# Kernel optimization log

Measured on AMD Instinct MI355X. Metric: run time of the kernel, lower is better.

Reference implementation:

```python
import jax, jax.numpy as jnp
import numpy as np

N = 100_000      # nodes
E = 1_600_000    # edges (avg degree 16)
H = 128          # hidden_channels == num_node_features
L = 6            # SAGEConv layers (third=True)
G = 128          # graphs in batch (for global_mean_pool)
C = 10           # num_classes
EPS = 1e-5       # BatchNorm eps


def setup_inputs() -> dict:
    key = jax.random.key(0)
    ks = jax.random.split(key, 8)
    s = 1.0 / np.sqrt(H)
    x = jax.random.normal(ks[0], (N, H), jnp.float32)
    edge_index = jax.random.randint(ks[1], (2, E), 0, N, dtype=jnp.int32)
    batch = jnp.sort(jax.random.randint(ks[2], (N,), 0, G, dtype=jnp.int32))
    return {
        "x": x,
        "edge_index": edge_index,
        "batch": batch,
        "Wl": jax.random.normal(ks[3], (L, H, H), jnp.float32) * s,  # neighbor lin
        "bl": jnp.zeros((L, H), jnp.float32),
        "Wr": jax.random.normal(ks[4], (L, H, H), jnp.float32) * s,  # root lin (no bias)
        "gamma": jnp.ones((L, H), jnp.float32),
        "beta": jnp.zeros((L, H), jnp.float32),
        "lin_W": jax.random.normal(ks[5], (H, C), jnp.float32) * s,
        "lin_b": jnp.zeros((C,), jnp.float32),
    }


def reference(x, edge_index, batch, Wl, bl, Wr, gamma, beta, lin_W, lin_b):
    src, dst = edge_index[0], edge_index[1]
    n = x.shape[0]
    # in-degree for mean aggregation (constant across layers)
    deg = jax.ops.segment_sum(jnp.ones((src.shape[0],), x.dtype), dst, num_segments=n)
    inv_deg = jnp.where(deg > 0, 1.0 / deg, 0.0)[:, None]  # [n,1]

    for l in range(Wl.shape[0]):
        # SAGEConv: lin_l(mean_{j->i} x_j) + lin_r(x_i)
        agg = jax.ops.segment_sum(x[src], dst, num_segments=n) * inv_deg  # [n,H]
        h = agg @ Wl[l] + bl[l] + x @ Wr[l]
        # BatchNorm1d (training-style batch stats, biased variance)
        mu = jnp.mean(h, axis=0)
        var = jnp.mean((h - mu) ** 2, axis=0)
        h = (h - mu) * jax.lax.rsqrt(var + EPS) * gamma[l] + beta[l]
        x = jax.nn.relu(h)

    # global_mean_pool over graph ids
    cnt = jax.ops.segment_sum(jnp.ones((n,), x.dtype), batch, num_segments=G)
    pooled = jax.ops.segment_sum(x, batch, num_segments=G) / jnp.maximum(cnt, 1.0)[:, None]
    # dropout(p=0.5) is identity in eval mode
    return pooled @ lin_W + lin_b  # [G, C]
```

## Files before the change

### kernel.cpp

```cpp
#include <hip/hip_runtime.h>
#include <hip/hip_bf16.h>

#define N_NODES 100000
#define N_EDGES 1600000
#define HDIM    128
#define NLAYER  6
#define NGRAPH  128
#define NCLASS  10
#define BN_EPS  1e-5f

#define POOL_SPLIT 16

#define NBUCK   196
#define BSH     9
#define KC_BLOCKS 250
#define KC_CHUNK  6400
#define LCOL_CAP  10240

#define GBM 128
#define NBLK_G ((N_NODES + GBM - 1) / GBM)

typedef __attribute__((ext_vector_type(8))) short short8v;
typedef __attribute__((ext_vector_type(4))) float f32x4;
typedef __attribute__((ext_vector_type(2))) float f32x2;
typedef __attribute__((ext_vector_type(4))) int int4v;
typedef __attribute__((ext_vector_type(2))) int int2v;

__device__ __forceinline__ float b2f(unsigned short h) {
    return __uint_as_float(((unsigned int)h) << 16);
}
__device__ __forceinline__ unsigned short f2b(float f) {
    unsigned int u = __float_as_uint(f);
    u += 0x7FFF + ((u >> 16) & 1);
    return (unsigned short)(u >> 16);
}
__device__ __forceinline__ void gl_lds16(const void* g, void* l) {
    __builtin_amdgcn_global_load_lds((const __attribute__((address_space(1))) unsigned int*)g,
                                     (__attribute__((address_space(3))) unsigned int*)l,
                                     16, 0, 0);
}
__device__ __forceinline__ short8v bn_pack(short8v v, float4 scA, float4 scB,
                                           float4 shA, float4 shB) {
    short8v o;
    o[0] = (short)f2b(fmaxf(0.f, b2f((unsigned short)v[0]) * scA.x + shA.x));
    o[1] = (short)f2b(fmaxf(0.f, b2f((unsigned short)v[1]) * scA.y + shA.y));
    o[2] = (short)f2b(fmaxf(0.f, b2f((unsigned short)v[2]) * scA.z + shA.z));
    o[3] = (short)f2b(fmaxf(0.f, b2f((unsigned short)v[3]) * scA.w + shA.w));
    o[4] = (short)f2b(fmaxf(0.f, b2f((unsigned short)v[4]) * scB.x + shB.x));
    o[5] = (short)f2b(fmaxf(0.f, b2f((unsigned short)v[5]) * scB.y + shB.y));
    o[6] = (short)f2b(fmaxf(0.f, b2f((unsigned short)v[6]) * scB.z + shB.z));
    o[7] = (short)f2b(fmaxf(0.f, b2f((unsigned short)v[7]) * scB.w + shB.w));
    return o;
}


__global__ void __launch_bounds__(256) k_hist(const int* __restrict__ dst,
                                              int* __restrict__ bcnt) {
    __shared__ int h[NBUCK];
    for (int i = threadIdx.x; i < NBUCK; i += 256) h[i] = 0;
    __syncthreads();
    const int4v* d4 = (const int4v*)dst;
    int base = blockIdx.x * (KC_CHUNK / 4);
    for (int i = threadIdx.x; i < KC_CHUNK / 4; i += 256) {
        int4v d = __builtin_nontemporal_load(d4 + base + i);
        atomicAdd(&h[d[0] >> BSH], 1);
        atomicAdd(&h[d[1] >> BSH], 1);
        atomicAdd(&h[d[2] >> BSH], 1);
        atomicAdd(&h[d[3] >> BSH], 1);
    }
    __syncthreads();
    for (int i = threadIdx.x; i < NBUCK; i += 256)
        if (h[i]) atomicAdd(&bcnt[i], h[i]);
}

__global__ void k_bscan(const int* __restrict__ bcnt, int* __restrict__ boff,
                        int* __restrict__ bcur, int* __restrict__ row_off) {
    if (threadIdx.x == 0 && blockIdx.x == 0) {
        int acc = 0;
        for (int i = 0; i < NBUCK; ++i) {
            boff[i] = acc; bcur[i] = acc; acc += bcnt[i];
        }
        boff[NBUCK] = acc;
        row_off[N_NODES] = N_EDGES;
    }
}

__global__ void __launch_bounds__(256) k_part(const int* __restrict__ src,
                                              const int* __restrict__ dst,
                                              int* __restrict__ bcur,
                                              int2v* __restrict__ P) {
    __shared__ int h[NBUCK];
    __shared__ int gbase[NBUCK];
    for (int i = threadIdx.x; i < NBUCK; i += 256) h[i] = 0;
    __syncthreads();
    const int4v* d4 = (const int4v*)dst;
    const int4v* s4 = (const int4v*)src;
    const int base = blockIdx.x * (KC_CHUNK / 4);
    for (int i = threadIdx.x; i < KC_CHUNK / 4; i += 256) {
        int4v d = __builtin_nontemporal_load(d4 + base + i);
        atomicAdd(&h[d[0] >> BSH], 1);
        atomicAdd(&h[d[1] >> BSH], 1);
        atomicAdd(&h[d[2] >> BSH], 1);
        atomicAdd(&h[d[3] >> BSH], 1);
    }
    __syncthreads();
    for (int i = threadIdx.x; i < NBUCK; i += 256) {
        int c = h[i];
        gbase[i] = c ? atomicAdd(&bcur[i], c) : 0;
        h[i] = 0;
    }
    __syncthreads();
    for (int i = threadIdx.x; i < KC_CHUNK / 4; i += 256) {
        int4v d = __builtin_nontemporal_load(d4 + base + i);
        int4v s = __builtin_nontemporal_load(s4 + base + i);
#pragma unroll
        for (int k = 0; k < 4; ++k) {
            int b = d[k] >> BSH;
            int pos = gbase[b] + atomicAdd(&h[b], 1);
            int2v pr; pr[0] = s[k]; pr[1] = d[k];
            P[pos] = pr;
        }
    }
}

__global__ void __launch_bounds__(1024) k_bucket(const int2v* __restrict__ P,
                                                 const int* __restrict__ boff,
                                                 int* __restrict__ row_off,
                                                 int* __restrict__ col) {
    __shared__ int ldeg[512];
    __shared__ int lcur[512];
    __shared__ int lcol[LCOL_CAP];
    const int tid = threadIdx.x;
    const int b = blockIdx.x;
    const int pbeg = boff[b], pend = boff[b + 1];
    const int nE = pend - pbeg;
    const int n0 = b << BSH;
    if (tid < 512) ldeg[tid] = 0;
    __syncthreads();
    for (int i = tid; i < nE; i += 1024) {
        int2v pr = P[pbeg + i];
        atomicAdd(&ldeg[pr[1] - n0], 1);
    }
    __syncthreads();
    int myd = (tid < 512) ? ldeg[tid] : 0;
    for (int off = 1; off < 512; off <<= 1) {
        int t = 0;
        if (tid < 512 && tid >= off) t = ldeg[tid - off];
        __syncthreads();
        if (tid < 512) ldeg[tid] += t;
        __syncthreads();
    }
    if (tid < 512) {
        int excl = ldeg[tid] - myd;
        lcur[tid] = excl;
        int node = n0 + tid;
        if (node < N_NODES) row_off[node] = pbeg + excl;
    }
    __syncthreads();
    for (int i = tid; i < nE; i += 1024) {
        int2v pr = P[pbeg + i];
        int pos = atomicAdd(&lcur[pr[1] - n0], 1);
        if (pos < LCOL_CAP) lcol[pos] = pr[0];
    }
    __syncthreads();
    for (int i = tid; i < nE; i += 1024) col[pbeg + i] = lcol[i];
}


__global__ void __launch_bounds__(256) k_cvt_x(const float* __restrict__ x,
                                               unsigned short* __restrict__ Xb,
                                               unsigned int* __restrict__ X8) {
    int idx = blockIdx.x * 256 + threadIdx.x;
    f32x4 v = __builtin_nontemporal_load(((const f32x4*)x) + idx);
    ushort4 o = { f2b(v[0]), f2b(v[1]), f2b(v[2]), f2b(v[3]) };
    ((ushort4*)Xb)[idx] = o;
    unsigned int d = 0;
    d = __builtin_amdgcn_cvt_pk_fp8_f32(v[0], v[1], d, false);
    d = __builtin_amdgcn_cvt_pk_fp8_f32(v[2], v[3], d, true);
    X8[idx] = d;
}

__global__ void __launch_bounds__(256) k_cvt_w(const float* __restrict__ Wl,
                                               const float* __restrict__ Wr,
                                               unsigned short* __restrict__ Wtb) {
    int idx = blockIdx.x * 256 + threadIdx.x;
    int kk = idx & 255;
    int n  = (idx >> 8) & 127;
    int l  = idx >> 15;
    float v = (kk < HDIM) ? Wl[l * HDIM * HDIM + kk * HDIM + n]
                          : Wr[l * HDIM * HDIM + (kk - HDIM) * HDIM + n];
    Wtb[idx] = f2b(v);
}

__global__ void __launch_bounds__(256) k_bnx8(const unsigned short* __restrict__ Hb,
                                              const float* __restrict__ scsh,
                                              int2v* __restrict__ X8) {
    int idx = blockIdx.x * 256 + threadIdx.x;
    int c8 = (idx & 15) * 8;
    short8v v = ((const short8v*)Hb)[idx];
    float f[8];
#pragma unroll
    for (int j = 0; j < 8; ++j)
        f[j] = fmaxf(0.f, b2f((unsigned short)v[j]) * scsh[c8 + j] + scsh[HDIM + c8 + j]);
    unsigned int d0 = 0, d1 = 0;
    d0 = __builtin_amdgcn_cvt_pk_fp8_f32(f[0], f[1], d0, false);
    d0 = __builtin_amdgcn_cvt_pk_fp8_f32(f[2], f[3], d0, true);
    d1 = __builtin_amdgcn_cvt_pk_fp8_f32(f[4], f[5], d1, false);
    d1 = __builtin_amdgcn_cvt_pk_fp8_f32(f[6], f[7], d1, true);
    int2v o; o[0] = (int)d0; o[1] = (int)d1;
    X8[idx] = o;
}


__global__ void __launch_bounds__(256) k_agg8(const unsigned char* __restrict__ X8,
                                              const int* __restrict__ row_off,
                                              const int* __restrict__ col,
                                              unsigned short* __restrict__ AGGb) {
    __shared__ int lcol[4096];
    __shared__ int sro[33];
    const int tid = threadIdx.x;
    const int nb0 = blockIdx.x * 32;
    if (tid <= 32) sro[tid] = row_off[nb0 + tid];
    __syncthreads();
    const int s0 = sro[0];
    const int nE = sro[32] - s0;
    const bool fits = (nE <= 4096);
    if (fits) {
        for (int i = tid; i < nE; i += 256) lcol[i] = col[s0 + i];
    }
    __syncthreads();

    const int g   = tid >> 3;
    const int c16 = (tid & 7) * 16;
    const int s = sro[g] - s0, e = sro[g + 1] - s0;
    const int* cp = fits ? lcol : (col + s0);

    f32x2 a2[8] = {};
    auto accum = [&](int4v v) {
#pragma unroll
        for (int q = 0; q < 4; ++q) {
            unsigned int w = (unsigned int)v[q];
            a2[2 * q]     += __builtin_amdgcn_cvt_pk_f32_fp8(w, false);
            a2[2 * q + 1] += __builtin_amdgcn_cvt_pk_f32_fp8(w, true);
        }
    };

    int p = s;
    for (; p + 8 <= e; p += 8) {
        int nbx[8];
#pragma unroll
        for (int j = 0; j < 8; ++j) nbx[j] = cp[p + j];
        int4v v[8];
#pragma unroll
        for (int j = 0; j < 8; ++j)
            v[j] = *(const int4v*)(X8 + (size_t)nbx[j] * HDIM + c16);
#pragma unroll
        for (int j = 0; j < 8; ++j) accum(v[j]);
    }
    if (p + 4 <= e) {
        int nbx[4];
#pragma unroll
        for (int j = 0; j < 4; ++j) nbx[j] = cp[p + j];
        int4v v[4];
#pragma unroll
        for (int j = 0; j < 4; ++j)
            v[j] = *(const int4v*)(X8 + (size_t)nbx[j] * HDIM + c16);
#pragma unroll
        for (int j = 0; j < 4; ++j) accum(v[j]);
        p += 4;
    }
    for (; p < e; ++p) {
        int4v v0 = *(const int4v*)(X8 + (size_t)cp[p] * HDIM + c16);
        accum(v0);
    }

    float w = (e > s) ? 1.0f / (float)(e - s) : 0.f;
    short8v o0, o1;
#pragma unroll
    for (int j = 0; j < 8; ++j) o0[j] = (short)f2b(a2[j >> 1][j & 1] * w);
#pragma unroll
    for (int j = 0; j < 8; ++j) o1[j] = (short)f2b(a2[4 + (j >> 1)][j & 1] * w);
    unsigned short* dst = AGGb + (size_t)(nb0 + g) * HDIM + c16;
    *(short8v*)dst = o0;
    *(short8v*)(dst + 8) = o1;
}


__global__ void __launch_bounds__(512) k_gemm_l0(const unsigned short* __restrict__ AGGb,
                                                 const unsigned short* __restrict__ Xb,
                                                 const unsigned short* __restrict__ Wtb,
                                                 const float* __restrict__ bl,
                                                 unsigned short* __restrict__ Hb,
                                                 float* __restrict__ pstat) {
    __shared__ __align__(16) char smem[32768];
    const int tid  = threadIdx.x;
    const int bm   = blockIdx.x * GBM;
    const int wv   = tid >> 6;
    const int lane = tid & 63;
    const int li   = lane & 15, hi = lane >> 4;
    const int wm   = wv & 1, wn = wv >> 1;

    f32x4 acc[4][2] = {};
    const int rr = tid >> 2, sk = tid & 3;
    const int swz = ((sk ^ ((rr >> 1) & 3)) << 4);

    auto stage = [&](int b, int step) {
        const unsigned short* Asrc = (step < 4) ? AGGb : Xb;
        const int kk0 = (step & 3) * 32;
        {
            int row = bm + rr; if (row >= N_NODES) row = N_NODES - 1;
            gl_lds16((const char*)(Asrc + (size_t)row * HDIM + kk0) + swz,
                     smem + b * 8192 + wv * 1024);
        }
        const int k0 = step * 32;
        gl_lds16((const char*)(Wtb + (size_t)rr * 256 + k0) + swz,
                 smem + 16384 + b * 8192 + wv * 1024);
    };

    stage(0, 0);
    __syncthreads();

    int buf = 0;
    for (int step = 0; step < 8; ++step) {
        if (step < 7) stage(buf ^ 1, step + 1);
        char* bA = smem + buf * 8192;
        char* bW = smem + 16384 + buf * 8192;
        short8v afr[4], bfr[2];
#pragma unroll
        for (int m = 0; m < 4; ++m) {
            int r = wm * 64 + m * 16 + li;
            afr[m] = *(const short8v*)(bA + r * 64 + ((hi ^ ((r >> 1) & 3)) << 4));
        }
#pragma unroll
        for (int nf = 0; nf < 2; ++nf) {
            int n = wn * 32 + nf * 16 + li;
            bfr[nf] = *(const short8v*)(bW + n * 64 + ((hi ^ ((n >> 1) & 3)) << 4));
        }
#pragma unroll
        for (int m = 0; m < 4; ++m)
#pragma unroll
            for (int nf = 0; nf < 2; ++nf)
                acc[m][nf] = __builtin_amdgcn_mfma_f32_16x16x32_bf16(afr[m], bfr[nf],
                                                                     acc[m][nf], 0, 0, 0);
        __syncthreads();
        buf ^= 1;
    }

    float* st = (float*)smem;
#pragma unroll
    for (int nf = 0; nf < 2; ++nf) {
        int c = wn * 32 + nf * 16 + li;
        float bb = bl[c];
        float ls = 0.f, lq = 0.f;
#pragma unroll
        for (int m = 0; m < 4; ++m) {
            int row0 = bm + wm * 64 + m * 16 + hi * 4;
#pragma unroll
            for (int j = 0; j < 4; ++j) {
                int row = row0 + j;
                if (row < N_NODES) {
                    float v = acc[m][nf][j] + bb;
                    Hb[(size_t)row * HDIM + c] = f2b(v);
                    ls += v; lq += v * v;
                }
            }
        }
        ls += __shfl_xor(ls, 16); ls += __shfl_xor(ls, 32);
        lq += __shfl_xor(lq, 16); lq += __shfl_xor(lq, 32);
        if (hi == 0) {
            st[wv * 128 + c] = ls;
            st[1024 + wv * 128 + c] = lq;
        }
    }
    __syncthreads();
    if (tid < 128) {
        int w0 = (tid >> 5) * 2;
        float s = st[w0 * 128 + tid] + st[(w0 + 1) * 128 + tid];
        pstat[blockIdx.x * 256 + tid] = s;
    } else if (tid < 256) {
        int c = tid - 128;
        int w0 = (c >> 5) * 2;
        float q = st[1024 + w0 * 128 + c] + st[1024 + (w0 + 1) * 128 + c];
        pstat[blockIdx.x * 256 + tid] = q;
    }
}

__global__ void __launch_bounds__(512) k_gemm_fuse(const unsigned short* __restrict__ AGGb,
                                                   const unsigned short* __restrict__ Hprev,
                                                   const float* __restrict__ scsh,
                                                   const unsigned short* __restrict__ Wtb,
                                                   const float* __restrict__ bl,
                                                   unsigned short* __restrict__ Hb,
                                                   float* __restrict__ pstat) {
    __shared__ __align__(16) char smem[32768];
    const int tid  = threadIdx.x;
    const int bm   = blockIdx.x * GBM;
    const int wv   = tid >> 6;
    const int lane = tid & 63;
    const int li   = lane & 15, hi = lane >> 4;
    const int wm   = wv & 1, wn = wv >> 1;

    f32x4 acc[4][2] = {};
    const int rr = tid >> 2, sk = tid & 3;
    const int swz = ((sk ^ ((rr >> 1) & 3)) << 4);

    auto stageW = [&](int b, int step) {
        const int k0 = step * 32;
        gl_lds16((const char*)(Wtb + (size_t)rr * 256 + k0) + swz,
                 smem + 16384 + b * 8192 + wv * 1024);
    };
    auto stageA = [&](int b, int step) {
        const int kk0 = step * 32;
        int row = bm + rr; if (row >= N_NODES) row = N_NODES - 1;
        gl_lds16((const char*)(AGGb + (size_t)row * HDIM + kk0) + swz,
                 smem + b * 8192 + wv * 1024);
    };

    stageA(0, 0); stageW(0, 0);
    __syncthreads();

    int buf = 0;
    for (int step = 0; step < 8; ++step) {
        char* curA = smem + buf * 8192;
        char* curW = smem + 16384 + buf * 8192;
        char* nxtA = smem + (buf ^ 1) * 8192;
        const int ns = step + 1;
        short8v rv;
        int c0 = 0;
        bool regstage = false;
        if (step < 7) {
            stageW(buf ^ 1, ns);
            if (ns < 4) {
                stageA(buf ^ 1, ns);
            } else {
                regstage = true;
                c0 = (ns - 4) * 32 + sk * 8;
                int row = bm + rr; if (row >= N_NODES) row = N_NODES - 1;
                rv = *(const short8v*)(Hprev + (size_t)row * HDIM + c0);
            }
        }

        short8v afr[4], bfr[2];
#pragma unroll
        for (int m = 0; m < 4; ++m) {
            int r = wm * 64 + m * 16 + li;
            afr[m] = *(const short8v*)(curA + r * 64 + ((hi ^ ((r >> 1) & 3)) << 4));
        }
#pragma unroll
        for (int nf = 0; nf < 2; ++nf) {
            int n = wn * 32 + nf * 16 + li;
            bfr[nf] = *(const short8v*)(curW + n * 64 + ((hi ^ ((n >> 1) & 3)) << 4));
        }
#pragma unroll
        for (int m = 0; m < 4; ++m)
#pragma unroll
            for (int nf = 0; nf < 2; ++nf)
                acc[m][nf] = __builtin_amdgcn_mfma_f32_16x16x32_bf16(afr[m], bfr[nf],
                                                                     acc[m][nf], 0, 0, 0);

        if (regstage) {
            float4 scA = *(const float4*)&scsh[c0];
            float4 scB = *(const float4*)&scsh[c0 + 4];
            float4 shA = *(const float4*)&scsh[HDIM + c0];
            float4 shB = *(const float4*)&scsh[HDIM + c0 + 4];
            *(short8v*)(nxtA + rr * 64 + swz) = bn_pack(rv, scA, scB, shA, shB);
        }
        __syncthreads();
        buf ^= 1;
    }

    float* st = (float*)smem;
#pragma unroll
    for (int nf = 0; nf < 2; ++nf) {
        int c = wn * 32 + nf * 16 + li;
        float bb = bl[c];
        float ls = 0.f, lq = 0.f;
#pragma unroll
        for (int m = 0; m < 4; ++m) {
            int row0 = bm + wm * 64 + m * 16 + hi * 4;
#pragma unroll
            for (int j = 0; j < 4; ++j) {
                int row = row0 + j;
                if (row < N_NODES) {
                    float v = acc[m][nf][j] + bb;
                    Hb[(size_t)row * HDIM + c] = f2b(v);
                    ls += v; lq += v * v;
                }
            }
        }
        ls += __shfl_xor(ls, 16); ls += __shfl_xor(ls, 32);
        lq += __shfl_xor(lq, 16); lq += __shfl_xor(lq, 32);
        if (hi == 0) {
            st[wv * 128 + c] = ls;
            st[1024 + wv * 128 + c] = lq;
        }
    }
    __syncthreads();
    if (tid < 128) {
        int w0 = (tid >> 5) * 2;
        float s = st[w0 * 128 + tid] + st[(w0 + 1) * 128 + tid];
        pstat[blockIdx.x * 256 + tid] = s;
    } else if (tid < 256) {
        int c = tid - 128;
        int w0 = (c >> 5) * 2;
        float q = st[1024 + w0 * 128 + c] + st[1024 + (w0 + 1) * 128 + c];
        pstat[blockIdx.x * 256 + tid] = q;
    }
}


__global__ void __launch_bounds__(256) k_red1(const float* __restrict__ pstat,
                                              float* __restrict__ red32) {
    int c = threadIdx.x, b = blockIdx.x;
    float s = 0.f;
    for (int r = b; r < NBLK_G; r += 32) s += pstat[r * 256 + c];
    red32[b * 256 + c] = s;
}

__global__ void __launch_bounds__(128) k_stats_final(const float* __restrict__ red32,
                                                     const float* __restrict__ gamma,
                                                     const float* __restrict__ beta,
                                                     float* __restrict__ scsh) {
    int c = threadIdx.x;
    float s = 0.f, q = 0.f;
    for (int r = 0; r < 32; ++r) { s += red32[r * 256 + c]; q += red32[r * 256 + 128 + c]; }
    float mu = s / (float)N_NODES;
    float var = q / (float)N_NODES - mu * mu;
    float rs = rsqrtf(var + BN_EPS);
    float sc = gamma[c] * rs;
    scsh[c] = sc;
    scsh[HDIM + c] = beta[c] - mu * sc;
}


__global__ void k_gbound(const int* __restrict__ batch, int* __restrict__ gb) {
    int t = blockIdx.x * 64 + threadIdx.x;
    if (t > NGRAPH) return;
    int lo = 0, hi = N_NODES;
    while (lo < hi) { int mid = (lo + hi) >> 1; if (batch[mid] < t) lo = mid + 1; else hi = mid; }
    gb[t] = lo;
}

__global__ void __launch_bounds__(128) k_pool_part(const unsigned short* __restrict__ Hb,
                                                   const float* __restrict__ scsh,
                                                   const int* __restrict__ gb,
                                                   float* __restrict__ ppart) {
    int g = blockIdx.x, sp = blockIdx.y;
    int c = threadIdx.x;
    float sc = scsh[c], sh = scsh[HDIM + c];
    int s = gb[g], e = gb[g + 1];
    float acc = 0.f;
    for (int i = s + sp; i < e; i += POOL_SPLIT)
        acc += fmaxf(0.f, b2f(Hb[(size_t)i * HDIM + c]) * sc + sh);
    ppart[(g * POOL_SPLIT + sp) * HDIM + c] = acc;
}

__global__ void __launch_bounds__(128) k_pool_final(const int* __restrict__ gb,
                                                    const float* __restrict__ ppart,
                                                    float* __restrict__ pooled) {
    int g = blockIdx.x, c = threadIdx.x;
    float s = 0.f;
    for (int sp = 0; sp < POOL_SPLIT; ++sp) s += ppart[(g * POOL_SPLIT + sp) * HDIM + c];
    int cnt = gb[g + 1] - gb[g]; if (cnt < 1) cnt = 1;
    pooled[g * HDIM + c] = s / (float)cnt;
}

__global__ void __launch_bounds__(128) k_lin(const float* __restrict__ pooled,
                                             const float* __restrict__ W,
                                             const float* __restrict__ bvec,
                                             float* __restrict__ out) {
    __shared__ float p[HDIM];
    int g = blockIdx.x, t = threadIdx.x;
    p[t] = pooled[g * HDIM + t];
    __syncthreads();
    if (t < NCLASS) {
        float acc = bvec[t];
        for (int k = 0; k < HDIM; ++k) acc += p[k] * W[k * NCLASS + t];
        out[g * NCLASS + t] = acc;
    }
}


extern "C" void kernel_launch(void* const* d_in, const int* in_sizes, int n_in,
                              void* d_out, int out_size, void* d_ws, size_t ws_size,
                              hipStream_t stream) {
    const float* x     = (const float*)d_in[0];
    const int*   eidx  = (const int*)d_in[1];
    const int*   batch = (const int*)d_in[2];
    const float* Wl    = (const float*)d_in[3];
    const float* bl    = (const float*)d_in[4];
    const float* Wr    = (const float*)d_in[5];
    const float* gamma = (const float*)d_in[6];
    const float* beta  = (const float*)d_in[7];
    const float* linW  = (const float*)d_in[8];
    const float* linb  = (const float*)d_in[9];
    float* out = (float*)d_out;

    const int* src = eidx;
    const int* dst = eidx + N_EDGES;

    char* p = (char*)d_ws;
    auto alloc = [&](size_t bytes) { char* r = p; p += (bytes + 255) & ~(size_t)255; return r; };
    unsigned short* Xb   = (unsigned short*)alloc((size_t)N_NODES * HDIM * 2);
    unsigned char*  X8   = (unsigned char*)alloc((size_t)N_NODES * HDIM);
    unsigned short* AGGb = (unsigned short*)alloc((size_t)N_NODES * HDIM * 2);
    unsigned short* HbA  = (unsigned short*)alloc((size_t)N_NODES * HDIM * 2);
    unsigned short* HbB  = (unsigned short*)alloc((size_t)N_NODES * HDIM * 2);
    unsigned short* Wtb  = (unsigned short*)alloc((size_t)NLAYER * 2 * HDIM * HDIM * 2);
    int*   row_off = (int*)alloc((N_NODES + 2) * 4);
    int*   col     = (int*)alloc((size_t)N_EDGES * 4);
    int2v* P       = (int2v*)alloc((size_t)N_EDGES * 8);
    int*   bcnt    = (int*)alloc(NBUCK * 4);
    int*   boff    = (int*)alloc((NBUCK + 1) * 4);
    int*   bcur    = (int*)alloc(NBUCK * 4);
    int*   gb      = (int*)alloc((NGRAPH + 2) * 4);
    float* pstat   = (float*)alloc((size_t)NBLK_G * 256 * 4);
    float* red32   = (float*)alloc(32 * 256 * 4);
    float* scsh    = (float*)alloc(2 * HDIM * 4);
    float* ppart   = (float*)alloc((size_t)NGRAPH * POOL_SPLIT * HDIM * 4);
    float* pooled  = (float*)alloc(NGRAPH * HDIM * 4);

    hipMemsetAsync(bcnt, 0, NBUCK * sizeof(int), stream);
    k_hist<<<KC_BLOCKS, 256, 0, stream>>>(dst, bcnt);
    k_bscan<<<1, 64, 0, stream>>>(bcnt, boff, bcur, row_off);
    k_part<<<KC_BLOCKS, 256, 0, stream>>>(src, dst, bcur, P);
    k_bucket<<<NBUCK, 1024, 0, stream>>>(P, boff, row_off, col);

    k_cvt_x<<<N_NODES * HDIM / 4 / 256, 256, 0, stream>>>(x, Xb, (unsigned int*)X8);
    k_cvt_w<<<NLAYER * 2 * HDIM * HDIM / 256, 256, 0, stream>>>(Wl, Wr, Wtb);
    k_gbound<<<3, 64, 0, stream>>>(batch, gb);

    k_agg8<<<N_NODES / 32, 256, 0, stream>>>(X8, row_off, col, AGGb);
    k_gemm_l0<<<NBLK_G, 512, 0, stream>>>(AGGb, Xb, Wtb, bl, HbA, pstat);
    k_red1<<<32, 256, 0, stream>>>(pstat, red32);
    k_stats_final<<<1, 128, 0, stream>>>(red32, gamma, beta, scsh);

    unsigned short* Hcur = HbA;
    for (int l = 1; l < NLAYER; ++l) {
        unsigned short* Hout = (l & 1) ? HbB : HbA;
        k_bnx8<<<N_NODES * HDIM / 8 / 256, 256, 0, stream>>>(Hcur, scsh, (int2v*)X8);
        k_agg8<<<N_NODES / 32, 256, 0, stream>>>(X8, row_off, col, AGGb);
        k_gemm_fuse<<<NBLK_G, 512, 0, stream>>>(
            AGGb, Hcur, scsh, Wtb + (size_t)l * 2 * HDIM * HDIM, bl + (size_t)l * HDIM,
            Hout, pstat);
        k_red1<<<32, 256, 0, stream>>>(pstat, red32);
        k_stats_final<<<1, 128, 0, stream>>>(red32, gamma + (size_t)l * HDIM,
                                             beta + (size_t)l * HDIM, scsh);
        Hcur = Hout;
    }

    k_pool_part<<<dim3(NGRAPH, POOL_SPLIT), 128, 0, stream>>>(Hcur, scsh, gb, ppart);
    k_pool_final<<<NGRAPH, 128, 0, stream>>>(gb, ppart, pooled);
    k_lin<<<NGRAPH, 128, 0, stream>>>(pooled, linW, linb, out);
}
```

Measured before the change: 560.9 us.

## Fuse neighbor aggregation into the SAGE GEMM kernel, drop the AGG buffer

Result: no change. 557.2 us (median of 2 runs) (-0.7%).

```diff
diff --git a/kernel.cpp b/kernel.cpp
--- a/kernel.cpp
+++ b/kernel.cpp
@@ -212,213 +212,90 @@
 }
 
 
-__global__ void __launch_bounds__(256) k_agg8(const unsigned char* __restrict__ X8,
-                                              const int* __restrict__ row_off,
-                                              const int* __restrict__ col,
-                                              unsigned short* __restrict__ AGGb) {
-    __shared__ int lcol[4096];
-    __shared__ int sro[33];
-    const int tid = threadIdx.x;
-    const int nb0 = blockIdx.x * 32;
-    if (tid <= 32) sro[tid] = row_off[nb0 + tid];
-    __syncthreads();
-    const int s0 = sro[0];
-    const int nE = sro[32] - s0;
-    const bool fits = (nE <= 4096);
-    if (fits) {
-        for (int i = tid; i < nE; i += 256) lcol[i] = col[s0 + i];
-    }
-    __syncthreads();
-
-    const int g   = tid >> 3;
-    const int c16 = (tid & 7) * 16;
-    const int s = sro[g] - s0, e = sro[g + 1] - s0;
-    const int* cp = fits ? lcol : (col + s0);
-
-    f32x2 a2[8] = {};
-    auto accum = [&](int4v v) {
-#pragma unroll
-        for (int q = 0; q < 4; ++q) {
-            unsigned int w = (unsigned int)v[q];
-            a2[2 * q]     += __builtin_amdgcn_cvt_pk_f32_fp8(w, false);
-            a2[2 * q + 1] += __builtin_amdgcn_cvt_pk_f32_fp8(w, true);
-        }
-    };
-
-    int p = s;
-    for (; p + 8 <= e; p += 8) {
-        int nbx[8];
-#pragma unroll
-        for (int j = 0; j < 8; ++j) nbx[j] = cp[p + j];
-        int4v v[8];
-#pragma unroll
-        for (int j = 0; j < 8; ++j)
-            v[j] = *(const int4v*)(X8 + (size_t)nbx[j] * HDIM + c16);
-#pragma unroll
-        for (int j = 0; j < 8; ++j) accum(v[j]);
-    }
-    if (p + 4 <= e) {
-        int nbx[4];
-#pragma unroll
-        for (int j = 0; j < 4; ++j) nbx[j] = cp[p + j];
-        int4v v[4];
-#pragma unroll
-        for (int j = 0; j < 4; ++j)
-            v[j] = *(const int4v*)(X8 + (size_t)nbx[j] * HDIM + c16);
-#pragma unroll
-        for (int j = 0; j < 4; ++j) accum(v[j]);
-        p += 4;
-    }
-    for (; p < e; ++p) {
-        int4v v0 = *(const int4v*)(X8 + (size_t)cp[p] * HDIM + c16);
-        accum(v0);
-    }
-
-    float w = (e > s) ? 1.0f / (float)(e - s) : 0.f;
-    short8v o0, o1;
-#pragma unroll
-    for (int j = 0; j < 8; ++j) o0[j] = (short)f2b(a2[j >> 1][j & 1] * w);
-#pragma unroll
-    for (int j = 0; j < 8; ++j) o1[j] = (short)f2b(a2[4 + (j >> 1)][j & 1] * w);
-    unsigned short* dst = AGGb + (size_t)(nb0 + g) * HDIM + c16;
-    *(short8v*)dst = o0;
-    *(short8v*)(dst + 8) = o1;
-}
-
-
-__global__ void __launch_bounds__(512) k_gemm_l0(const unsigned short* __restrict__ AGGb,
-                                                 const unsigned short* __restrict__ Xb,
-                                                 const unsigned short* __restrict__ Wtb,
-                                                 const float* __restrict__ bl,
-                                                 unsigned short* __restrict__ Hb,
-                                                 float* __restrict__ pstat) {
+template<bool BN>
+__global__ void __launch_bounds__(512) k_fused(const unsigned char* __restrict__ X8,
+                                               const unsigned short* __restrict__ Hprev,
+                                               const float* __restrict__ scsh,
+                                               const int* __restrict__ row_off,
+                                               const int* __restrict__ col,
+                                               const unsigned short* __restrict__ Wtb,
+                                               const float* __restrict__ bl,
+                                               unsigned short* __restrict__ Hb,
+                                               float* __restrict__ pstat) {
     __shared__ __align__(16) char smem[32768];
+    __shared__ int sro[129];
     const int tid  = threadIdx.x;
     const int bm   = blockIdx.x * GBM;
     const int wv   = tid >> 6;
     const int lane = tid & 63;
     const int li   = lane & 15, hi = lane >> 4;
     const int wm   = wv & 1, wn = wv >> 1;
+    const int rr   = tid >> 2, sk = tid & 3;
+    const int swz  = ((sk ^ ((rr >> 1) & 3)) << 4);
+
+    gl_lds16((const char*)(Wtb + (size_t)rr * 256) + swz, smem + 16384 + wv * 1024);
+
+    int* lcol = (int*)smem;
+    if (tid <= 128) {
+        int ii = bm + tid; if (ii > N_NODES) ii = N_NODES;
+        sro[tid] = row_off[ii];
+    }
+    __syncthreads();
+    const int s0 = sro[0];
+    const int nEb = sro[128] - s0;
+    const bool fits = (nEb <= 4096);
+    if (fits) for (int i = tid; i < nEb; i += 512) lcol[i] = col[s0 + i];
+    __syncthreads();
+
+    const int s = sro[rr] - s0, e = sro[rr + 1] - s0;
+    const int* cp = fits ? lcol : (col + s0);
+    const int c32 = sk * 32;
+    f32x2 a2[16] = {};
+    auto accum16 = [&](int4v v, int base) {
+#pragma unroll
+        for (int q = 0; q < 4; ++q) {
+            unsigned int w = (unsigned int)v[q];
+            a2[base + 2 * q]     += __builtin_amdgcn_cvt_pk_f32_fp8(w, false);
+            a2[base + 2 * q + 1] += __builtin_amdgcn_cvt_pk_f32_fp8(w, true);
+        }
+    };
+    int p = s;
+    for (; p + 4 <= e; p += 4) {
+        int nbx[4];
+#pragma unroll
+        for (int j = 0; j < 4; ++j) nbx[j] = cp[p + j];
+        int4v v0[4], v1[4];
+#pragma unroll
+        for (int j = 0; j < 4; ++j) {
+            const unsigned char* rowp = X8 + (size_t)nbx[j] * HDIM + c32;
+            v0[j] = *(const int4v*)rowp;
+            v1[j] = *(const int4v*)(rowp + 16);
+        }
+#pragma unroll
+        for (int j = 0; j < 4; ++j) { accum16(v0[j], 0); accum16(v1[j], 8); }
+    }
+    for (; p < e; ++p) {
+        const unsigned char* rowp = X8 + (size_t)cp[p] * HDIM + c32;
+        accum16(*(const int4v*)rowp, 0);
+        accum16(*(const int4v*)(rowp + 16), 8);
+    }
+    const float wgt = (e > s) ? 1.0f / (float)(e - s) : 0.f;
+    short8v aggout[4];
+#pragma unroll
+    for (int j = 0; j < 4; ++j)
+#pragma unroll
+        for (int t = 0; t < 8; ++t)
+            aggout[j][t] = (short)f2b(a2[j * 4 + (t >> 1)][t & 1] * wgt);
+
+    __syncthreads();
+    if (sk == 0) {
+#pragma unroll
+        for (int j = 0; j < 4; ++j)
+            *(short8v*)(smem + rr * 64 + ((j ^ ((rr >> 1) & 3)) << 4)) = aggout[j];
+    }
+    __syncthreads();
 
     f32x4 acc[4][2] = {};
-    const int rr = tid >> 2, sk = tid & 3;
-    const int swz = ((sk ^ ((rr >> 1) & 3)) << 4);
-
-    auto stage = [&](int b, int step) {
-        const unsigned short* Asrc = (step < 4) ? AGGb : Xb;
-        const int kk0 = (step & 3) * 32;
-        {
-            int row = bm + rr; if (row >= N_NODES) row = N_NODES - 1;
-            gl_lds16((const char*)(Asrc + (size_t)row * HDIM + kk0) + swz,
-                     smem + b * 8192 + wv * 1024);
-        }
-        const int k0 = step * 32;
-        gl_lds16((const char*)(Wtb + (size_t)rr * 256 + k0) + swz,
-                 smem + 16384 + b * 8192 + wv * 1024);
-    };
-
-    stage(0, 0);
-    __syncthreads();
-
-    int buf = 0;
-    for (int step = 0; step < 8; ++step) {
-        if (step < 7) stage(buf ^ 1, step + 1);
-        char* bA = smem + buf * 8192;
-        char* bW = smem + 16384 + buf * 8192;
-        short8v afr[4], bfr[2];
-#pragma unroll
-        for (int m = 0; m < 4; ++m) {
-            int r = wm * 64 + m * 16 + li;
-            afr[m] = *(const short8v*)(bA + r * 64 + ((hi ^ ((r >> 1) & 3)) << 4));
-        }
-#pragma unroll
-        for (int nf = 0; nf < 2; ++nf) {
-            int n = wn * 32 + nf * 16 + li;
-            bfr[nf] = *(const short8v*)(bW + n * 64 + ((hi ^ ((n >> 1) & 3)) << 4));
-        }
-#pragma unroll
-        for (int m = 0; m < 4; ++m)
-#pragma unroll
-            for (int nf = 0; nf < 2; ++nf)
-                acc[m][nf] = __builtin_amdgcn_mfma_f32_16x16x32_bf16(afr[m], bfr[nf],
-                                                                     acc[m][nf], 0, 0, 0);
-        __syncthreads();
-        buf ^= 1;
-    }
-
-    float* st = (float*)smem;
-#pragma unroll
-    for (int nf = 0; nf < 2; ++nf) {
-        int c = wn * 32 + nf * 16 + li;
-        float bb = bl[c];
-        float ls = 0.f, lq = 0.f;
-#pragma unroll
-        for (int m = 0; m < 4; ++m) {
-            int row0 = bm + wm * 64 + m * 16 + hi * 4;
-#pragma unroll
-            for (int j = 0; j < 4; ++j) {
-                int row = row0 + j;
-                if (row < N_NODES) {
-                    float v = acc[m][nf][j] + bb;
-                    Hb[(size_t)row * HDIM + c] = f2b(v);
-                    ls += v; lq += v * v;
-                }
-            }
-        }
-        ls += __shfl_xor(ls, 16); ls += __shfl_xor(ls, 32);
-        lq += __shfl_xor(lq, 16); lq += __shfl_xor(lq, 32);
-        if (hi == 0) {
-            st[wv * 128 + c] = ls;
-            st[1024 + wv * 128 + c] = lq;
-        }
-    }
-    __syncthreads();
-    if (tid < 128) {
-        int w0 = (tid >> 5) * 2;
-        float s = st[w0 * 128 + tid] + st[(w0 + 1) * 128 + tid];
-        pstat[blockIdx.x * 256 + tid] = s;
-    } else if (tid < 256) {
-        int c = tid - 128;
-        int w0 = (c >> 5) * 2;
-        float q = st[1024 + w0 * 128 + c] + st[1024 + (w0 + 1) * 128 + c];
-        pstat[blockIdx.x * 256 + tid] = q;
-    }
-}
-
-__global__ void __launch_bounds__(512) k_gemm_fuse(const unsigned short* __restrict__ AGGb,
-                                                   const unsigned short* __restrict__ Hprev,
-                                                   const float* __restrict__ scsh,
-                                                   const unsigned short* __restrict__ Wtb,
-                                                   const float* __restrict__ bl,
-                                                   unsigned short* __restrict__ Hb,
-                                                   float* __restrict__ pstat) {
-    __shared__ __align__(16) char smem[32768];
-    const int tid  = threadIdx.x;
-    const int bm   = blockIdx.x * GBM;
-    const int wv   = tid >> 6;
-    const int lane = tid & 63;
-    const int li   = lane & 15, hi = lane >> 4;
-    const int wm   = wv & 1, wn = wv >> 1;
-
-    f32x4 acc[4][2] = {};
-    const int rr = tid >> 2, sk = tid & 3;
-    const int swz = ((sk ^ ((rr >> 1) & 3)) << 4);
-
-    auto stageW = [&](int b, int step) {
-        const int k0 = step * 32;
-        gl_lds16((const char*)(Wtb + (size_t)rr * 256 + k0) + swz,
-                 smem + 16384 + b * 8192 + wv * 1024);
-    };
-    auto stageA = [&](int b, int step) {
-        const int kk0 = step * 32;
-        int row = bm + rr; if (row >= N_NODES) row = N_NODES - 1;
-        gl_lds16((const char*)(AGGb + (size_t)row * HDIM + kk0) + swz,
-                 smem + b * 8192 + wv * 1024);
-    };
-
-    stageA(0, 0); stageW(0, 0);
-    __syncthreads();
-
     int buf = 0;
     for (int step = 0; step < 8; ++step) {
         char* curA = smem + buf * 8192;
@@ -429,10 +306,9 @@
         int c0 = 0;
         bool regstage = false;
         if (step < 7) {
-            stageW(buf ^ 1, ns);
-            if (ns < 4) {
-                stageA(buf ^ 1, ns);
-            } else {
+            gl_lds16((const char*)(Wtb + (size_t)rr * 256 + ns * 32) + swz,
+                     smem + 16384 + (buf ^ 1) * 8192 + wv * 1024);
+            if (ns >= 4) {
                 regstage = true;
                 c0 = (ns - 4) * 32 + sk * 8;
                 int row = bm + rr; if (row >= N_NODES) row = N_NODES - 1;
@@ -458,12 +334,26 @@
                 acc[m][nf] = __builtin_amdgcn_mfma_f32_16x16x32_bf16(afr[m], bfr[nf],
                                                                      acc[m][nf], 0, 0, 0);
 
-        if (regstage) {
-            float4 scA = *(const float4*)&scsh[c0];
-            float4 scB = *(const float4*)&scsh[c0 + 4];
-            float4 shA = *(const float4*)&scsh[HDIM + c0];
-            float4 shB = *(const float4*)&scsh[HDIM + c0 + 4];
-            *(short8v*)(nxtA + rr * 64 + swz) = bn_pack(rv, scA, scB, shA, shB);
+        if (step < 7) {
+            if (ns < 4) {
+                if (sk == ns) {
+#pragma unroll
+                    for (int j = 0; j < 4; ++j)
+                        *(short8v*)(nxtA + rr * 64 + ((j ^ ((rr >> 1) & 3)) << 4)) = aggout[j];
+                }
+            } else {
+                short8v ov;
+                if (BN) {
+                    float4 scA = *(const float4*)&scsh[c0];
+                    float4 scB = *(const float4*)&scsh[c0 + 4];
+                    float4 shA = *(const float4*)&scsh[HDIM + c0];
+                    float4 shB = *(const float4*)&scsh[HDIM + c0 + 4];
+                    ov = bn_pack(rv, scA, scB, shA, shB);
+                } else {
+                    ov = rv;
+                }
+                *(short8v*)(nxtA + rr * 64 + swz) = ov;
+            }
         }
         __syncthreads();
         buf ^= 1;
@@ -498,8 +388,8 @@
     __syncthreads();
     if (tid < 128) {
         int w0 = (tid >> 5) * 2;
-        float s = st[w0 * 128 + tid] + st[(w0 + 1) * 128 + tid];
-        pstat[blockIdx.x * 256 + tid] = s;
+        float s2 = st[w0 * 128 + tid] + st[(w0 + 1) * 128 + tid];
+        pstat[blockIdx.x * 256 + tid] = s2;
     } else if (tid < 256) {
         int c = tid - 128;
         int w0 = (c >> 5) * 2;
@@ -603,7 +493,6 @@
     auto alloc = [&](size_t bytes) { char* r = p; p += (bytes + 255) & ~(size_t)255; return r; };
     unsigned short* Xb   = (unsigned short*)alloc((size_t)N_NODES * HDIM * 2);
     unsigned char*  X8   = (unsigned char*)alloc((size_t)N_NODES * HDIM);
-    unsigned short* AGGb = (unsigned short*)alloc((size_t)N_NODES * HDIM * 2);
     unsigned short* HbA  = (unsigned short*)alloc((size_t)N_NODES * HDIM * 2);
     unsigned short* HbB  = (unsigned short*)alloc((size_t)N_NODES * HDIM * 2);
     unsigned short* Wtb  = (unsigned short*)alloc((size_t)NLAYER * 2 * HDIM * HDIM * 2);
@@ -630,8 +519,8 @@
     k_cvt_w<<<NLAYER * 2 * HDIM * HDIM / 256, 256, 0, stream>>>(Wl, Wr, Wtb);
     k_gbound<<<3, 64, 0, stream>>>(batch, gb);
 
-    k_agg8<<<N_NODES / 32, 256, 0, stream>>>(X8, row_off, col, AGGb);
-    k_gemm_l0<<<NBLK_G, 512, 0, stream>>>(AGGb, Xb, Wtb, bl, HbA, pstat);
+    k_fused<false><<<NBLK_G, 512, 0, stream>>>(X8, Xb, scsh, row_off, col,
+                                               Wtb, bl, HbA, pstat);
     k_red1<<<32, 256, 0, stream>>>(pstat, red32);
     k_stats_final<<<1, 128, 0, stream>>>(red32, gamma, beta, scsh);
 
@@ -639,10 +528,9 @@
     for (int l = 1; l < NLAYER; ++l) {
         unsigned short* Hout = (l & 1) ? HbB : HbA;
         k_bnx8<<<N_NODES * HDIM / 8 / 256, 256, 0, stream>>>(Hcur, scsh, (int2v*)X8);
-        k_agg8<<<N_NODES / 32, 256, 0, stream>>>(X8, row_off, col, AGGb);
-        k_gemm_fuse<<<NBLK_G, 512, 0, stream>>>(
-            AGGb, Hcur, scsh, Wtb + (size_t)l * 2 * HDIM * HDIM, bl + (size_t)l * HDIM,
-            Hout, pstat);
+        k_fused<true><<<NBLK_G, 512, 0, stream>>>(
+            X8, Hcur, scsh, row_off, col, Wtb + (size_t)l * 2 * HDIM * HDIM,
+            bl + (size_t)l * HDIM, Hout, pstat);
         k_red1<<<32, 256, 0, stream>>>(pstat, red32);
         k_stats_final<<<1, 128, 0, stream>>>(red32, gamma + (size_t)l * HDIM,
                                              beta + (size_t)l * HDIM, scsh);
```
